# Kernel optimization log

Hardware: AMD Instinct MI355X
Metric: run time of the kernel (lower is better)

## Reference

```python
import jax, jax.numpy as jnp
import numpy as np

L, C, H, FF = 12, 768, 12, 3072
DH = C // H
VOCAB = 30522
B, P, T = 64, 196, 40
PATCH_FLAT = 768  # 16*16*3
MAXP, MAXW = P + 1, T + 2


def _ln(x, w, b, eps):
    m = jnp.mean(x, axis=-1, keepdims=True)
    v = jnp.mean(jnp.square(x - m), axis=-1, keepdims=True)
    return (x - m) * jax.lax.rsqrt(v + eps) * w + b


def setup_inputs() -> dict:
    key = jax.random.key(0)
    ks = iter(jax.random.split(key, 40))
    s = 0.02
    rn = lambda shape: jax.random.normal(next(ks), shape, jnp.float32) * s
    return {
        'vis_in': jax.random.normal(next(ks), (B, P, PATCH_FLAT), jnp.float32),
        'txt_in': jax.random.randint(next(ks), (B, T), 0, VOCAB),
        'vis_mask': jnp.ones((B, P), jnp.int32),
        'txt_mask': jnp.ones((B, T), jnp.int32),
        'patch_w': rn((C, PATCH_FLAT)), 'patch_b': jnp.zeros((C,), jnp.float32),
        'w_embed': rn((VOCAB, C)),
        't_pos': rn((MAXW, C)),
        'v_pos': rn((1, MAXP, C)),
        'v_cls': rn((1, 1, C)),
        'v_mod': rn((1, 1, C)), 't_mod': rn((1, 1, C)),
        'vn_w': jnp.ones((C,), jnp.float32), 'vn_b': jnp.zeros((C,), jnp.float32),
        'tn_w': jnp.ones((C,), jnp.float32), 'tn_b': jnp.zeros((C,), jnp.float32),
        'qkv_w': rn((L, 3 * C, C)), 'qkv_b': jnp.zeros((L, 3 * C), jnp.float32),
        'proj_w': rn((L, C, C)), 'proj_b': jnp.zeros((L, C), jnp.float32),
        'n1_w': jnp.ones((L, C), jnp.float32), 'n1_b': jnp.zeros((L, C), jnp.float32),
        'n2_w': jnp.ones((L, C), jnp.float32), 'n2_b': jnp.zeros((L, C), jnp.float32),
        'fc1_w': rn((L, FF, C)), 'fc1_b': jnp.zeros((L, FF), jnp.float32),
        'fc2_w': rn((L, C, FF)), 'fc2_b': jnp.zeros((L, C), jnp.float32),
    }


def reference(vis_in, txt_in, vis_mask, txt_mask, patch_w, patch_b, w_embed, t_pos,
              v_pos, v_cls, v_mod, t_mod, vn_w, vn_b, tn_w, tn_b, qkv_w, qkv_b,
              proj_w, proj_b, n1_w, n1_b, n2_w, n2_b, fc1_w, fc1_b, fc2_w, fc2_b):
    Bsz = vis_in.shape[0]
    # patch projection and word embedding
    v_emb = vis_in @ patch_w.T + patch_b                      # [B, P, C]
    t_emb = w_embed[txt_in]                                    # [B, T, C]
    v_emb = jnp.concatenate([jnp.broadcast_to(v_cls, (Bsz, 1, C)), v_emb], axis=1)
    VL = v_emb.shape[1]                                        # P + 1
    v_emb = _ln(v_emb + v_pos[:, :VL] + v_mod, vn_w, vn_b, 1e-5)
    t_emb = _ln(t_emb + t_pos[:T] + t_mod, tn_w, tn_b, 1e-5)
    x = jnp.concatenate([t_emb, v_emb], axis=1)                # [B, N, C], N = T+1+P
    m = jnp.concatenate([txt_mask, jnp.ones((Bsz, 1), txt_mask.dtype), vis_mask], axis=-1)
    # pairwise mask: attn_mask[b,i,j] == 0 -> masked (broadcast over heads)
    masked = (m[:, None, :, None] * m[:, None, None, :]) == 0  # [B,1,N,N]
    scale = DH ** -0.5
    for l in range(L):
        h = _ln(x, n1_w[l], n1_b[l], 1e-6)
        qkv = (h @ qkv_w[l].T + qkv_b[l]).reshape(Bsz, -1, 3, H, DH)
        q = jnp.transpose(qkv[:, :, 0], (0, 2, 1, 3))          # [B,H,N,DH]
        k = jnp.transpose(qkv[:, :, 1], (0, 2, 1, 3))
        v = jnp.transpose(qkv[:, :, 2], (0, 2, 1, 3))
        attn = jnp.einsum('bhqd,bhkd->bhqk', q, k) * scale
        attn = jnp.where(masked, jnp.asarray(-1e30, attn.dtype), attn)
        attn = jax.nn.softmax(attn, axis=-1)
        o = jnp.einsum('bhqk,bhkd->bhqd', attn, v)
        o = jnp.transpose(o, (0, 2, 1, 3)).reshape(Bsz, -1, C)
        x = x + (o @ proj_w[l].T + proj_b[l])
        h2 = _ln(x, n2_w[l], n2_b[l], 1e-6)
        h2 = jax.nn.gelu(h2 @ fc1_w[l].T + fc1_b[l], approximate=False)
        x = x + (h2 @ fc2_w[l].T + fc2_b[l])
    return x
```

## Files before the change

### kernel.cpp

```cpp
#include <hip/hip_runtime.h>
#include <hip/hip_bf16.h>

using bf16 = __hip_bfloat16;
typedef __bf16 bfv8 __attribute__((ext_vector_type(8)));
typedef float f32x4 __attribute__((ext_vector_type(4)));

#define DEVI __device__ __forceinline__

constexpr int L_ = 12, C_ = 768, H_ = 12, FF_ = 3072, DH_ = 64;
constexpr int B_ = 64, P_ = 196, T_ = 40;
constexpr int N_ = T_ + 1 + P_;
constexpr int M_ = B_ * N_;
constexpr int MPAD = 15360;
constexpr int NKV = 256;
constexpr int BP_ = B_ * P_;

constexpr size_t OFF_X   = 0;
constexpr size_t SZ_X    = (size_t)MPAD * C_ * 4;
constexpr size_t OFF_H   = OFF_X + SZ_X;
constexpr size_t SZ_H    = (size_t)MPAD * C_ * 2;
constexpr size_t OFF_Q   = OFF_H + SZ_H;
constexpr size_t SZ_QKV1 = (size_t)B_ * H_ * NKV * DH_ * 2;
constexpr size_t OFF_K   = OFF_Q + SZ_QKV1;
constexpr size_t OFF_V   = OFF_K + SZ_QKV1;
constexpr size_t OFF_O   = OFF_V + SZ_QKV1;
constexpr size_t SZ_O    = SZ_H;
constexpr size_t OFF_FFH = OFF_O + SZ_O;
constexpr size_t SZ_FFH  = (size_t)MPAD * FF_ * 2;
constexpr size_t OFF_WB  = OFF_FFH + SZ_FFH;
constexpr size_t SZ_WB   = (size_t)(2304 + 768 + 3072 + 3072) * 768 * 2;
constexpr size_t WS_NEED = OFF_WB + SZ_WB;
constexpr size_t OFF_PTMP = OFF_FFH;
constexpr size_t OFF_VISB = OFF_FFH + (size_t)40 * 1024 * 1024;
constexpr size_t OFF_PWB  = OFF_WB;

DEVI void gld_lds16(const bf16* g, bf16* l) {
  __builtin_amdgcn_global_load_lds((__attribute__((address_space(1))) void*)(g),
                                   (__attribute__((address_space(3))) void*)(l), 16, 0, 0);
}

DEVI void swz_tiles(int bid, int G, int NTC, int& bm, int& bn) {
  const int qq = G >> 3, rr = G & 7;
  const int xcd = bid & 7, base = bid >> 3;
  const int lin = (xcd < rr ? xcd * (qq + 1) : rr * (qq + 1) + (xcd - rr) * qq) + base;
  bm = lin / NTC;
  bn = lin - bm * NTC;
}

DEVI uint packbf(float lo, float hi) {
  union { struct { bf16 x, y; } h; uint u; } r;
  r.h.x = __float2bfloat16(lo); r.h.y = __float2bfloat16(hi);
  return r.u;
}

DEVI float gelu_f(float v) {
  const float p = v * (1.5957691f + 0.07135481f * v * v) * 1.442695041f;
  const float d = exp2f(-p);
  return v / (1.f + d);
}

template <int EPI>
__global__ __launch_bounds__(256) void gemm_mb(
    const bf16* __restrict__ A, const bf16* __restrict__ W,
    const float* __restrict__ bias, float* __restrict__ outf,
    float* __restrict__ outf2, bf16* __restrict__ outb,
    bf16* __restrict__ qb, bf16* __restrict__ kb, bf16* __restrict__ vb,
    int Nout, int K, int Mvalid, int NTC) {
  __shared__ alignas(16) bf16 As[2][128 * 32];
  __shared__ alignas(16) bf16 Bs[2][128 * 32];

  const int tid = threadIdx.x, wid = tid >> 6, lane = tid & 63;
  const int wm = wid >> 1, wn = wid & 1;
  int bm, bn;
  swz_tiles(blockIdx.x, gridDim.x, NTC, bm, bn);
  const size_t arow0 = (size_t)bm * 128;
  const size_t brow0 = (size_t)bn * 128;

  const int srow = tid >> 2;
  const int gch = ((tid & 3) - ((tid >> 3) & 3)) & 3;
  const bf16* pa0 = A + (arow0 + srow) * K + gch * 8;
  const bf16* pa1 = A + (arow0 + 64 + srow) * K + gch * 8;
  const bf16* pb0 = W + (brow0 + srow) * K + gch * 8;
  const bf16* pb1 = W + (brow0 + 64 + srow) * K + gch * 8;
  bf16* da0[2] = {&As[0][(wid * 16) * 32], &As[1][(wid * 16) * 32]};
  bf16* da1[2] = {&As[0][(64 + wid * 16) * 32], &As[1][(64 + wid * 16) * 32]};
  bf16* db0[2] = {&Bs[0][(wid * 16) * 32], &Bs[1][(wid * 16) * 32]};
  bf16* db1[2] = {&Bs[0][(64 + wid * 16) * 32], &Bs[1][(64 + wid * 16) * 32]};

  auto STAGE = [&](int t, int b) {
    const size_t k = (size_t)t * 32;
    gld_lds16(pa0 + k, da0[b]);
    gld_lds16(pa1 + k, da1[b]);
    gld_lds16(pb0 + k, db0[b]);
    gld_lds16(pb1 + k, db1[b]);
  };

  f32x4 acc[4][4];
#pragma unroll
  for (int m = 0; m < 4; m++)
#pragma unroll
    for (int n = 0; n < 4; n++) acc[m][n] = (f32x4){0.f, 0.f, 0.f, 0.f};

  const int la = lane & 15, g = lane >> 4;
  const int slot8 = ((g + (la >> 1)) & 3) * 8;

  const int NT = K >> 5;
  STAGE(0, 0);
  for (int t = 0; t < NT; ++t) {
    const int b = t & 1;
    if (t + 1 < NT) {
      STAGE(t + 1, b ^ 1);
      asm volatile("s_waitcnt vmcnt(4)" ::: "memory");
    } else {
      asm volatile("s_waitcnt vmcnt(0)" ::: "memory");
    }
    asm volatile("s_barrier" ::: "memory");
    bfv8 af[4], bfr[4];
#pragma unroll
    for (int n = 0; n < 4; n++)
      bfr[n] = *(const bfv8*)&Bs[b][(wn * 64 + n * 16 + la) * 32 + slot8];
#pragma unroll
    for (int m = 0; m < 4; m++)
      af[m] = *(const bfv8*)&As[b][(wm * 64 + m * 16 + la) * 32 + slot8];
#pragma unroll
    for (int m = 0; m < 4; m++)
#pragma unroll
      for (int n = 0; n < 4; n++)
        acc[m][n] = __builtin_amdgcn_mfma_f32_16x16x32_bf16(af[m], bfr[n], acc[m][n], 0, 0, 0);
    asm volatile("s_barrier" ::: "memory");
  }

  const int row0 = (int)arow0 + wm * 64;
  const int col0 = (int)brow0 + wn * 64;
  float bv[4];
#pragma unroll
  for (int n = 0; n < 4; n++) bv[n] = bias[col0 + n * 16 + la];

  if constexpr (EPI == 0 || EPI == 2 || EPI == 4) {
#pragma unroll
    for (int n = 0; n < 4; n++) {
      const int colb = col0 + n * 16 + la;
#pragma unroll
      for (int m = 0; m < 4; m++)
#pragma unroll
        for (int j = 0; j < 4; j++) {
          const int row = row0 + m * 16 + g * 4 + j;
          const float v = acc[m][n][j] + bv[n];
          if constexpr (EPI == 0) outf[(size_t)row * Nout + colb] = v;
          else if constexpr (EPI == 2) outf[(size_t)row * Nout + colb] += v;
          else { if (row < Mvalid) outf2[(size_t)row * Nout + colb] = outf[(size_t)row * Nout + colb] + v; }
        }
    }
  } else if constexpr (EPI == 3) {
#pragma unroll
    for (int m = 0; m < 4; m++)
#pragma unroll
      for (int j = 0; j < 4; j++) {
        const int row = row0 + m * 16 + g * 4 + j;
#pragma unroll
        for (int n = 0; n < 4; n++) {
          const float v = gelu_f(acc[m][n][j] + bv[n]);
          const float p = __shfl_xor(v, 1);
          if (!(lane & 1))
            *(uint*)(outb + (size_t)row * Nout + col0 + n * 16 + la) = packbf(v, p);
        }
      }
  } else {
#pragma unroll
    for (int m = 0; m < 4; m++)
#pragma unroll
      for (int j = 0; j < 4; j++) {
        const int row = row0 + m * 16 + g * 4 + j;
        const bool ok = row < Mvalid;
        const int bI = row / N_;
        const int nI = row - bI * N_;
#pragma unroll
        for (int n = 0; n < 4; n++) {
          const int colb = col0 + n * 16 + la;
          const float v = acc[m][n][j] + bv[n];
          const float p = __shfl_xor(v, 1);
          if (ok && !(lane & 1)) {
            const int s = colb / C_;
            const int rem = colb - s * C_;
            const int hh = rem >> 6, dd = rem & 63;
            bf16* dst = (s == 0) ? qb : (s == 1) ? kb : vb;
            *(uint*)(dst + (((size_t)bI * H_ + hh) * NKV + nI) * DH_ + dd) = packbf(v, p);
          }
        }
      }
  }
}

__global__ __launch_bounds__(256) void conv_weights_k(
    const float* __restrict__ wq, const float* __restrict__ wp,
    const float* __restrict__ wf1, const float* __restrict__ wf2,
    bf16* __restrict__ dst) {
  const long n0 = 2304L * 768 / 4, n1 = 768L * 768 / 4;
  const long n2 = 3072L * 768 / 4;
  const long tot = n0 + n1 + 2 * n2;
  for (long i = (long)blockIdx.x * 256 + threadIdx.x; i < tot; i += (long)gridDim.x * 256) {
    const float* s; long off;
    if (i < n0) { s = wq; off = i; }
    else if (i < n0 + n1) { s = wp; off = i - n0; }
    else if (i < n0 + n1 + n2) { s = wf1; off = i - n0 - n1; }
    else { s = wf2; off = i - n0 - n1 - n2; }
    float4 v = ((const float4*)s)[off];
    union { short4 q; bf16 h[4]; } u;
    u.h[0] = __float2bfloat16(v.x); u.h[1] = __float2bfloat16(v.y);
    u.h[2] = __float2bfloat16(v.z); u.h[3] = __float2bfloat16(v.w);
    ((short4*)dst)[i] = u.q;
  }
}

__global__ __launch_bounds__(256) void f32_to_bf16_k(const float* __restrict__ s,
                                                     bf16* __restrict__ d, long n4) {
  long i = (long)blockIdx.x * 256 + threadIdx.x;
  long stride = (long)gridDim.x * 256;
  for (; i < n4; i += stride) {
    float4 v = ((const float4*)s)[i];
    union { short4 q; bf16 h[4]; } u;
    u.h[0] = __float2bfloat16(v.x); u.h[1] = __float2bfloat16(v.y);
    u.h[2] = __float2bfloat16(v.z); u.h[3] = __float2bfloat16(v.w);
    ((short4*)d)[i] = u.q;
  }
}

__global__ __launch_bounds__(256) void embed_kernel(
    const float* __restrict__ ptmp, const int* __restrict__ txt_in,
    const float* __restrict__ wemb, const float* __restrict__ tpos,
    const float* __restrict__ vpos, const float* __restrict__ vcls,
    const float* __restrict__ vmod, const float* __restrict__ tmod,
    const float* __restrict__ vnw, const float* __restrict__ vnb,
    const float* __restrict__ tnw, const float* __restrict__ tnb,
    float* __restrict__ x) {
  const int row = blockIdx.x;
  const int tid = threadIdx.x;
  if (row >= M_) {
    for (int i = tid; i < C_; i += 256) x[(size_t)row * C_ + i] = 0.f;
    return;
  }
  const int b = row / N_, n = row - (row / N_) * N_;
  const bool istxt = n < T_;
  float e[3];
#pragma unroll
  for (int i = 0; i < 3; i++) {
    const int c = tid + i * 256;
    float v;
    if (istxt) {
      v = wemb[(size_t)txt_in[b * T_ + n] * C_ + c] + tpos[n * C_ + c] + tmod[c];
    } else {
      const int vi = n - T_;
      const float base = (vi == 0) ? vcls[c] : ptmp[((size_t)b * P_ + (vi - 1)) * C_ + c];
      v = base + vpos[vi * C_ + c] + vmod[c];
    }
    e[i] = v;
  }
  float s = e[0] + e[1] + e[2];
  float s2 = e[0] * e[0] + e[1] * e[1] + e[2] * e[2];
#pragma unroll
  for (int d = 1; d < 64; d <<= 1) { s += __shfl_xor(s, d); s2 += __shfl_xor(s2, d); }
  __shared__ float rs[4], rs2[4];
  const int wid = tid >> 6, lane = tid & 63;
  if (lane == 0) { rs[wid] = s; rs2[wid] = s2; }
  __syncthreads();
  s = rs[0] + rs[1] + rs[2] + rs[3];
  s2 = rs2[0] + rs2[1] + rs2[2] + rs2[3];
  const float mean = s * (1.f / C_);
  const float var = s2 * (1.f / C_) - mean * mean;
  const float rr = rsqrtf(var + 1e-5f);
  const float* w = istxt ? tnw : vnw;
  const float* bb = istxt ? tnb : vnb;
#pragma unroll
  for (int i = 0; i < 3; i++) {
    const int c = tid + i * 256;
    x[(size_t)row * C_ + c] = (e[i] - mean) * rr * w[c] + bb[c];
  }
}

__global__ __launch_bounds__(256) void ln_rows(const float* __restrict__ x,
                                               const float* __restrict__ w,
                                               const float* __restrict__ b,
                                               bf16* __restrict__ out, float eps) {
  const int row = blockIdx.x * 4 + (threadIdx.x >> 6);
  const int lane = threadIdx.x & 63;
  if (row >= MPAD) return;
  bf16* op = out + (size_t)row * C_;
  if (row >= M_) {
#pragma unroll
    for (int i = 0; i < 3; i++)
      *(short4*)(op + (lane + 64 * i) * 4) = make_short4(0, 0, 0, 0);
    return;
  }
  const float4* xp = (const float4*)(x + (size_t)row * C_);
  float4 v[3];
  float s = 0.f, s2 = 0.f;
#pragma unroll
  for (int i = 0; i < 3; i++) {
    v[i] = xp[lane + 64 * i];
    s += v[i].x + v[i].y + v[i].z + v[i].w;
    s2 += v[i].x * v[i].x + v[i].y * v[i].y + v[i].z * v[i].z + v[i].w * v[i].w;
  }
#pragma unroll
  for (int d = 1; d < 64; d <<= 1) { s += __shfl_xor(s, d); s2 += __shfl_xor(s2, d); }
  const float mean = s * (1.f / C_);
  const float rr = rsqrtf(s2 * (1.f / C_) - mean * mean + eps);
#pragma unroll
  for (int i = 0; i < 3; i++) {
    const int c0 = (lane + 64 * i) * 4;
    const float4 w4 = *(const float4*)(w + c0);
    const float4 b4 = *(const float4*)(b + c0);
    union { short4 s4; bf16 h[4]; } u;
    u.h[0] = __float2bfloat16((v[i].x - mean) * rr * w4.x + b4.x);
    u.h[1] = __float2bfloat16((v[i].y - mean) * rr * w4.y + b4.y);
    u.h[2] = __float2bfloat16((v[i].z - mean) * rr * w4.z + b4.z);
    u.h[3] = __float2bfloat16((v[i].w - mean) * rr * w4.w + b4.w);
    *(short4*)(op + c0) = u.s4;
  }
}

DEVI float maskval(const int* __restrict__ tm, const int* __restrict__ vm, int b, int j) {
  if (j < T_) return tm[b * T_ + j] ? 1.f : 0.f;
  if (j == T_) return 1.f;
  if (j < N_) return vm[b * P_ + (j - T_ - 1)] ? 1.f : 0.f;
  return 0.f;
}

__global__ __launch_bounds__(256) void attn_fused(
    const bf16* __restrict__ qb, const bf16* __restrict__ kb,
    const bf16* __restrict__ vb, const int* __restrict__ txt_mask,
    const int* __restrict__ vis_mask, bf16* __restrict__ ob) {
  __shared__ alignas(16) __bf16 Vt[64 * 264];
  __shared__ alignas(16) __bf16 Ps[64 * 264];
  const int qblk = blockIdx.x;
  const int bh = blockIdx.y;
  const int b = bh / H_, hh = bh - b * H_;
  const int tid = threadIdx.x, wid = tid >> 6, lane = tid & 63;

  const __bf16* Vg = (const __bf16*)(vb + (size_t)bh * NKV * DH_);
#pragma unroll
  for (int it = 0; it < 8; it++) {
    const int r = lane + 64 * (it & 3);
    const int c8 = (wid + 4 * (it >> 2)) * 8;
    bfv8 v;
    if (r < N_) v = *(const bfv8*)(Vg + (size_t)r * DH_ + c8);
    else { union { int4 i; bfv8 x; } z; z.i = make_int4(0,0,0,0); v = z.x; }
#pragma unroll
    for (int d = 0; d < 8; d++) Vt[(c8 + d) * 264 + r] = v[d];
  }

  const int qbase = qblk * 64 + wid * 16;
  const __bf16* Qg = (const __bf16*)(qb + (size_t)bh * NKV * DH_);
  const __bf16* Kg = (const __bf16*)(kb + (size_t)bh * NKV * DH_);
  bfv8 aq[2];
#pragma unroll
  for (int kk = 0; kk < 2; kk++)
    aq[kk] = *(const bfv8*)(Qg + (size_t)(qbase + (lane & 15)) * DH_ + kk * 32 + (lane >> 4) * 8);

  f32x4 acc[16];
#pragma unroll
  for (int f = 0; f < 16; f++) acc[f] = (f32x4){0.f, 0.f, 0.f, 0.f};
#pragma unroll
  for (int f = 0; f < 16; f++) {
#pragma unroll
    for (int kk = 0; kk < 2; kk++) {
      bfv8 bk = *(const bfv8*)(Kg + (size_t)(f * 16 + (lane & 15)) * DH_ + kk * 32 + (lane >> 4) * 8);
      acc[f] = __builtin_amdgcn_mfma_f32_16x16x32_bf16(aq[kk], bk, acc[f], 0, 0, 0);
    }
  }

  float cm[16];
#pragma unroll
  for (int f = 0; f < 16; f++)
    cm[f] = maskval(txt_mask, vis_mask, b, f * 16 + (lane & 15));

  const float scale = 0.125f;
#pragma unroll
  for (int j = 0; j < 4; j++) {
    const int qr = qbase + (lane >> 4) * 4 + j;
    const float qm = (qr < N_) ? maskval(txt_mask, vis_mask, b, qr) : 1.f;
    float sv[16];
    float mx = -3.0e38f;
#pragma unroll
    for (int f = 0; f < 16; f++) {
      const int col = f * 16 + (lane & 15);
      float sc;
      if (col >= N_) sc = -INFINITY;
      else if (qm * cm[f] == 0.f) sc = -1e30f;
      else sc = acc[f][j] * scale;
      sv[f] = sc;
      mx = fmaxf(mx, sc);
    }
#pragma unroll
    for (int d = 1; d < 16; d <<= 1) mx = fmaxf(mx, __shfl_xor(mx, d));
    float sum = 0.f;
#pragma unroll
    for (int f = 0; f < 16; f++) { const float p = expf(sv[f] - mx); sv[f] = p; sum += p; }
#pragma unroll
    for (int d = 1; d < 16; d <<= 1) sum += __shfl_xor(sum, d);
    const float inv = 1.f / sum;
    const int ql = wid * 16 + (lane >> 4) * 4 + j;
#pragma unroll
    for (int f = 0; f < 16; f++)
      Ps[ql * 264 + f * 16 + (lane & 15)] = (__bf16)(sv[f] * inv);
  }

  __syncthreads();

  f32x4 oacc[4];
#pragma unroll
  for (int n = 0; n < 4; n++) oacc[n] = (f32x4){0.f, 0.f, 0.f, 0.f};
#pragma unroll
  for (int kk = 0; kk < 8; kk++) {
    bfv8 ap = *(const bfv8*)&Ps[(wid * 16 + (lane & 15)) * 264 + kk * 32 + (lane >> 4) * 8];
#pragma unroll
    for (int n = 0; n < 4; n++) {
      bfv8 bv = *(const bfv8*)&Vt[(n * 16 + (lane & 15)) * 264 + kk * 32 + (lane >> 4) * 8];
      oacc[n] = __builtin_amdgcn_mfma_f32_16x16x32_bf16(ap, bv, oacc[n], 0, 0, 0);
    }
  }
#pragma unroll
  for (int n = 0; n < 4; n++)
#pragma unroll
    for (int j = 0; j < 4; j++) {
      const int q = qbase + (lane >> 4) * 4 + j;
      if (q < N_)
        ob[((size_t)b * N_ + q) * C_ + hh * 64 + n * 16 + (lane & 15)] =
            __float2bfloat16(oacc[n][j]);
    }
}

extern "C" void kernel_launch(void* const* d_in, const int* in_sizes, int n_in,
                              void* d_out, int out_size, void* d_ws, size_t ws_size,
                              hipStream_t stream) {
  const float* vis_in  = (const float*)d_in[0];
  const int*   txt_in  = (const int*)d_in[1];
  const int*   vis_mask = (const int*)d_in[2];
  const int*   txt_mask = (const int*)d_in[3];
  const float* patch_w = (const float*)d_in[4];
  const float* patch_b = (const float*)d_in[5];
  const float* w_embed = (const float*)d_in[6];
  const float* t_pos   = (const float*)d_in[7];
  const float* v_pos   = (const float*)d_in[8];
  const float* v_cls   = (const float*)d_in[9];
  const float* v_mod   = (const float*)d_in[10];
  const float* t_mod   = (const float*)d_in[11];
  const float* vn_w = (const float*)d_in[12];
  const float* vn_b = (const float*)d_in[13];
  const float* tn_w = (const float*)d_in[14];
  const float* tn_b = (const float*)d_in[15];
  const float* qkv_w = (const float*)d_in[16];
  const float* qkv_b = (const float*)d_in[17];
  const float* proj_w = (const float*)d_in[18];
  const float* proj_b = (const float*)d_in[19];
  const float* n1_w = (const float*)d_in[20];
  const float* n1_b = (const float*)d_in[21];
  const float* n2_w = (const float*)d_in[22];
  const float* n2_b = (const float*)d_in[23];
  const float* fc1_w = (const float*)d_in[24];
  const float* fc1_b = (const float*)d_in[25];
  const float* fc2_w = (const float*)d_in[26];
  const float* fc2_b = (const float*)d_in[27];

  char* ws = (char*)d_ws;
  if (ws_size < WS_NEED) {
    hipMemsetAsync(d_out, 0, (size_t)out_size * 4, stream);
    return;
  }
  float* x    = (float*)(ws + OFF_X);
  bf16* h     = (bf16*)(ws + OFF_H);
  bf16* qbuf  = (bf16*)(ws + OFF_Q);
  bf16* kbuf  = (bf16*)(ws + OFF_K);
  bf16* vbuf  = (bf16*)(ws + OFF_V);
  bf16* obuf  = (bf16*)(ws + OFF_O);
  bf16* ffh   = (bf16*)(ws + OFF_FFH);
  bf16* wq    = (bf16*)(ws + OFF_WB);
  bf16* wp    = wq + (size_t)2304 * 768;
  bf16* wf1   = wp + (size_t)768 * 768;
  bf16* wf2   = wf1 + (size_t)3072 * 768;
  float* ptmp = (float*)(ws + OFF_PTMP);
  bf16* visb  = (bf16*)(ws + OFF_VISB);
  bf16* pwb   = (bf16*)(ws + OFF_PWB);

  f32_to_bf16_k<<<1024, 256, 0, stream>>>(vis_in, visb, (long)BP_ * C_ / 4);
  f32_to_bf16_k<<<256, 256, 0, stream>>>(patch_w, pwb, (long)C_ * C_ / 4);
  gemm_mb<0><<<(BP_ / 128) * (C_ / 128), 256, 0, stream>>>(
      visb, pwb, patch_b, ptmp, nullptr, nullptr, nullptr, nullptr, nullptr,
      C_, C_, BP_, C_ / 128);
  embed_kernel<<<MPAD, 256, 0, stream>>>(ptmp, txt_in, w_embed, t_pos, v_pos, v_cls,
                                         v_mod, t_mod, vn_w, vn_b, tn_w, tn_b, x);

  for (int l = 0; l < L_; l++) {
    conv_weights_k<<<2048, 256, 0, stream>>>(
        qkv_w + (size_t)l * 2304 * 768, proj_w + (size_t)l * 768 * 768,
        fc1_w + (size_t)l * 3072 * 768, fc2_w + (size_t)l * 768 * 3072, wq);

    ln_rows<<<MPAD / 4, 256, 0, stream>>>(x, n1_w + l * C_, n1_b + l * C_, h, 1e-6f);
    gemm_mb<1><<<(MPAD / 128) * (2304 / 128), 256, 0, stream>>>(
        h, wq, qkv_b + (size_t)l * 2304, nullptr, nullptr, nullptr, qbuf, kbuf, vbuf,
        2304, C_, M_, 2304 / 128);
    attn_fused<<<dim3(4, B_ * H_), 256, 0, stream>>>(qbuf, kbuf, vbuf, txt_mask,
                                                     vis_mask, obuf);
    gemm_mb<2><<<(MPAD / 128) * (C_ / 128), 256, 0, stream>>>(
        obuf, wp, proj_b + (size_t)l * C_, x, nullptr, nullptr, nullptr, nullptr,
        nullptr, C_, C_, M_, C_ / 128);
    ln_rows<<<MPAD / 4, 256, 0, stream>>>(x, n2_w + l * C_, n2_b + l * C_, h, 1e-6f);
    gemm_mb<3><<<(MPAD / 128) * (FF_ / 128), 256, 0, stream>>>(
        h, wf1, fc1_b + (size_t)l * FF_, nullptr, nullptr, ffh, nullptr, nullptr,
        nullptr, FF_, C_, M_, FF_ / 128);
    if (l < L_ - 1) {
      gemm_mb<2><<<(MPAD / 128) * (C_ / 128), 256, 0, stream>>>(
          ffh, wf2, fc2_b + (size_t)l * C_, x, nullptr, nullptr, nullptr, nullptr,
          nullptr, C_, FF_, M_, C_ / 128);
    } else {
      gemm_mb<4><<<(MPAD / 128) * (C_ / 128), 256, 0, stream>>>(
          ffh, wf2, fc2_b + (size_t)l * C_, x, (float*)d_out, nullptr, nullptr,
          nullptr, nullptr, C_, FF_, M_, C_ / 128);
    }
  }
}
```

Before: 6.019 ms.

## Replace 128x128 GEMM with 256x256 8-wave pipelined tile kernel

```diff
diff --git a/kernel.cpp b/kernel.cpp
--- a/kernel.cpp
+++ b/kernel.cpp
@@ -60,77 +60,118 @@
 }
 
 template <int EPI>
-__global__ __launch_bounds__(256) void gemm_mb(
+__global__ __launch_bounds__(512, 2) void gemm8q(
     const bf16* __restrict__ A, const bf16* __restrict__ W,
     const float* __restrict__ bias, float* __restrict__ outf,
     float* __restrict__ outf2, bf16* __restrict__ outb,
     bf16* __restrict__ qb, bf16* __restrict__ kb, bf16* __restrict__ vb,
     int Nout, int K, int Mvalid, int NTC) {
-  __shared__ alignas(16) bf16 As[2][128 * 32];
-  __shared__ alignas(16) bf16 Bs[2][128 * 32];
+  extern __shared__ __align__(16) char lds[];
+  constexpr int BUFSZ = 65536;
+  constexpr int BOFF  = 32768;
 
   const int tid = threadIdx.x, wid = tid >> 6, lane = tid & 63;
-  const int wm = wid >> 1, wn = wid & 1;
+  const int wm = wid >> 2, wn = wid & 3;
   int bm, bn;
   swz_tiles(blockIdx.x, gridDim.x, NTC, bm, bn);
-  const size_t arow0 = (size_t)bm * 128;
-  const size_t brow0 = (size_t)bn * 128;
-
-  const int srow = tid >> 2;
-  const int gch = ((tid & 3) - ((tid >> 3) & 3)) & 3;
-  const bf16* pa0 = A + (arow0 + srow) * K + gch * 8;
-  const bf16* pa1 = A + (arow0 + 64 + srow) * K + gch * 8;
-  const bf16* pb0 = W + (brow0 + srow) * K + gch * 8;
-  const bf16* pb1 = W + (brow0 + 64 + srow) * K + gch * 8;
-  bf16* da0[2] = {&As[0][(wid * 16) * 32], &As[1][(wid * 16) * 32]};
-  bf16* da1[2] = {&As[0][(64 + wid * 16) * 32], &As[1][(64 + wid * 16) * 32]};
-  bf16* db0[2] = {&Bs[0][(wid * 16) * 32], &Bs[1][(wid * 16) * 32]};
-  bf16* db1[2] = {&Bs[0][(64 + wid * 16) * 32], &Bs[1][(64 + wid * 16) * 32]};
-
-  auto STAGE = [&](int t, int b) {
-    const size_t k = (size_t)t * 32;
-    gld_lds16(pa0 + k, da0[b]);
-    gld_lds16(pa1 + k, da1[b]);
-    gld_lds16(pb0 + k, db0[b]);
-    gld_lds16(pb1 + k, db1[b]);
+  const size_t arow0 = (size_t)bm * 256;
+  const size_t brow0 = (size_t)bn * 256;
+
+  const int lrow = lane >> 3;
+  const int xr = ((lane & 7) ^ lrow) * 8;
+  const bf16* Ag = A + (arow0 + wid * 16 + lrow) * K + xr;
+  const bf16* Wg = W + (brow0 + wid * 16 + lrow) * K + xr;
+
+  auto STG = [&](int isA, int h, int t, int P) {
+    char* base = lds + P * BUFSZ + (isA ? 0 : BOFF) + h * 16384 + wid * 2048;
+    const bf16* g = (isA ? Ag : Wg) + (size_t)(h * 128) * K + t * 64;
+    gld_lds16(g, (bf16*)base);
+    gld_lds16(g + (size_t)8 * K, (bf16*)(base + 1024));
   };
 
-  f32x4 acc[4][4];
-#pragma unroll
-  for (int m = 0; m < 4; m++)
+  const int la = lane & 15, g4 = lane >> 4;
+  const int s7 = lane & 7;
+
+  f32x4 acc[8][4];
+#pragma unroll
+  for (int m = 0; m < 8; m++)
 #pragma unroll
     for (int n = 0; n < 4; n++) acc[m][n] = (f32x4){0.f, 0.f, 0.f, 0.f};
 
-  const int la = lane & 15, g = lane >> 4;
-  const int slot8 = ((g + (la >> 1)) & 3) * 8;
-
-  const int NT = K >> 5;
-  STAGE(0, 0);
-  for (int t = 0; t < NT; ++t) {
-    const int b = t & 1;
-    if (t + 1 < NT) {
-      STAGE(t + 1, b ^ 1);
-      asm volatile("s_waitcnt vmcnt(4)" ::: "memory");
-    } else {
-      asm volatile("s_waitcnt vmcnt(0)" ::: "memory");
-    }
-    asm volatile("s_barrier" ::: "memory");
-    bfv8 af[4], bfr[4];
-#pragma unroll
-    for (int n = 0; n < 4; n++)
-      bfr[n] = *(const bfv8*)&Bs[b][(wn * 64 + n * 16 + la) * 32 + slot8];
-#pragma unroll
-    for (int m = 0; m < 4; m++)
-      af[m] = *(const bfv8*)&As[b][(wm * 64 + m * 16 + la) * 32 + slot8];
-#pragma unroll
-    for (int m = 0; m < 4; m++)
-#pragma unroll
-      for (int n = 0; n < 4; n++)
-        acc[m][n] = __builtin_amdgcn_mfma_f32_16x16x32_bf16(af[m], bfr[n], acc[m][n], 0, 0, 0);
-    asm volatile("s_barrier" ::: "memory");
-  }
-
-  const int row0 = (int)arow0 + wm * 64;
+  bfv8 af[4][2], bfr[4][2];
+
+  auto DSRA = [&](int P, int mo) {
+    const char* ab = lds + P * BUFSZ + wm * 16384;
+#pragma unroll
+    for (int mi = 0; mi < 4; mi++) {
+      const int r = (mo + mi) * 16 + la;
+#pragma unroll
+      for (int ks = 0; ks < 2; ks++)
+        af[mi][ks] = *(const bfv8*)(ab + r * 128 + (((ks * 4 + g4) ^ s7) * 16));
+    }
+  };
+  auto DSRB = [&](int P, int no) {
+    const char* bb = lds + P * BUFSZ + BOFF + (wn >> 1) * 16384;
+#pragma unroll
+    for (int ni = 0; ni < 2; ni++) {
+      const int c = (wn & 1) * 64 + (no + ni) * 16 + la;
+#pragma unroll
+      for (int ks = 0; ks < 2; ks++)
+        bfr[no + ni][ks] = *(const bfv8*)(bb + c * 128 + (((ks * 4 + g4) ^ s7) * 16));
+    }
+  };
+  auto QM = [&](int mo, int no) {
+    __builtin_amdgcn_s_setprio(1);
+#pragma unroll
+    for (int ks = 0; ks < 2; ks++)
+#pragma unroll
+      for (int mi = 0; mi < 4; mi++)
+#pragma unroll
+        for (int ni = 0; ni < 2; ni++)
+          acc[mo + mi][no + ni] = __builtin_amdgcn_mfma_f32_16x16x32_bf16(
+              af[mi][ks], bfr[no + ni][ks], acc[mo + mi][no + ni], 0, 0, 0);
+    __builtin_amdgcn_s_setprio(0);
+  };
+
+#define BARR asm volatile("s_barrier" ::: "memory")
+
+  const int NT = K >> 6;
+  const int NI = NT >> 1;
+
+  STG(1, 0, 0, 0); STG(1, 1, 0, 0); STG(0, 0, 0, 0); STG(0, 1, 0, 0);
+  STG(0, 0, 1, 1); STG(0, 1, 1, 1);
+  asm volatile("s_waitcnt vmcnt(4)" ::: "memory");
+  BARR;
+
+  for (int i = 0; i < NI; i++) {
+    const int t = 2 * i;
+    const bool p2 = (t + 2 < NT), p3 = (t + 3 < NT);
+    DSRA(0, 0); DSRB(0, 0); STG(1, 0, t + 1, 1);
+    BARR; QM(0, 0); BARR;
+    DSRB(0, 2); STG(1, 1, t + 1, 1);
+    BARR; QM(0, 2); BARR;
+    DSRA(0, 4); if (p2) STG(0, 0, t + 2, 0);
+    BARR; QM(4, 0); BARR;
+    if (p2) STG(0, 1, t + 2, 0);
+    BARR; QM(4, 2);
+    if (p2) { asm volatile("s_waitcnt vmcnt(4)" ::: "memory"); }
+    else    { asm volatile("s_waitcnt vmcnt(0)" ::: "memory"); }
+    BARR;
+    DSRA(1, 0); DSRB(1, 0); if (p2) STG(1, 0, t + 2, 0);
+    BARR; QM(0, 0); BARR;
+    DSRB(1, 2); if (p2) STG(1, 1, t + 2, 0);
+    BARR; QM(0, 2); BARR;
+    DSRA(1, 4); if (p3) STG(0, 0, t + 3, 1);
+    BARR; QM(4, 0); BARR;
+    if (p3) STG(0, 1, t + 3, 1);
+    BARR; QM(4, 2);
+    if (p3) { asm volatile("s_waitcnt vmcnt(4)" ::: "memory"); }
+    else    { asm volatile("s_waitcnt vmcnt(0)" ::: "memory"); }
+    BARR;
+  }
+#undef BARR
+
+  const int row0 = (int)arow0 + wm * 128;
   const int col0 = (int)brow0 + wn * 64;
   float bv[4];
 #pragma unroll
@@ -141,10 +182,10 @@
     for (int n = 0; n < 4; n++) {
       const int colb = col0 + n * 16 + la;
 #pragma unroll
-      for (int m = 0; m < 4; m++)
+      for (int m = 0; m < 8; m++)
 #pragma unroll
         for (int j = 0; j < 4; j++) {
-          const int row = row0 + m * 16 + g * 4 + j;
+          const int row = row0 + m * 16 + g4 * 4 + j;
           const float v = acc[m][n][j] + bv[n];
           if constexpr (EPI == 0) outf[(size_t)row * Nout + colb] = v;
           else if constexpr (EPI == 2) outf[(size_t)row * Nout + colb] += v;
@@ -153,10 +194,10 @@
     }
   } else if constexpr (EPI == 3) {
 #pragma unroll
-    for (int m = 0; m < 4; m++)
+    for (int m = 0; m < 8; m++)
 #pragma unroll
       for (int j = 0; j < 4; j++) {
-        const int row = row0 + m * 16 + g * 4 + j;
+        const int row = row0 + m * 16 + g4 * 4 + j;
 #pragma unroll
         for (int n = 0; n < 4; n++) {
           const float v = gelu_f(acc[m][n][j] + bv[n]);
@@ -167,10 +208,10 @@
       }
   } else {
 #pragma unroll
-    for (int m = 0; m < 4; m++)
+    for (int m = 0; m < 8; m++)
 #pragma unroll
       for (int j = 0; j < 4; j++) {
-        const int row = row0 + m * 16 + g * 4 + j;
+        const int row = row0 + m * 16 + g4 * 4 + j;
         const bool ok = row < Mvalid;
         const int bI = row / N_;
         const int nI = row - bI * N_;
@@ -481,11 +522,18 @@
   bf16* visb  = (bf16*)(ws + OFF_VISB);
   bf16* pwb   = (bf16*)(ws + OFF_PWB);
 
+  constexpr int LDSQ = 131072;
+  (void)hipFuncSetAttribute((const void*)gemm8q<0>, hipFuncAttributeMaxDynamicSharedMemorySize, LDSQ);
+  (void)hipFuncSetAttribute((const void*)gemm8q<1>, hipFuncAttributeMaxDynamicSharedMemorySize, LDSQ);
+  (void)hipFuncSetAttribute((const void*)gemm8q<2>, hipFuncAttributeMaxDynamicSharedMemorySize, LDSQ);
+  (void)hipFuncSetAttribute((const void*)gemm8q<3>, hipFuncAttributeMaxDynamicSharedMemorySize, LDSQ);
+  (void)hipFuncSetAttribute((const void*)gemm8q<4>, hipFuncAttributeMaxDynamicSharedMemorySize, LDSQ);
+
   f32_to_bf16_k<<<1024, 256, 0, stream>>>(vis_in, visb, (long)BP_ * C_ / 4);
   f32_to_bf16_k<<<256, 256, 0, stream>>>(patch_w, pwb, (long)C_ * C_ / 4);
-  gemm_mb<0><<<(BP_ / 128) * (C_ / 128), 256, 0, stream>>>(
+  gemm8q<0><<<(BP_ / 256) * (C_ / 256), 512, LDSQ, stream>>>(
       visb, pwb, patch_b, ptmp, nullptr, nullptr, nullptr, nullptr, nullptr,
-      C_, C_, BP_, C_ / 128);
+      C_, C_, BP_, C_ / 256);
   embed_kernel<<<MPAD, 256, 0, stream>>>(ptmp, txt_in, w_embed, t_pos, v_pos, v_cls,
                                          v_mod, t_mod, vn_w, vn_b, tn_w, tn_b, x);
 
@@ -495,26 +543,26 @@
         fc1_w + (size_t)l * 3072 * 768, fc2_w + (size_t)l * 768 * 3072, wq);
 
     ln_rows<<<MPAD / 4, 256, 0, stream>>>(x, n1_w + l * C_, n1_b + l * C_, h, 1e-6f);
-    gemm_mb<1><<<(MPAD / 128) * (2304 / 128), 256, 0, stream>>>(
+    gemm8q<1><<<(MPAD / 256) * (2304 / 256), 512, LDSQ, stream>>>(
         h, wq, qkv_b + (size_t)l * 2304, nullptr, nullptr, nullptr, qbuf, kbuf, vbuf,
-        2304, C_, M_, 2304 / 128);
+        2304, C_, M_, 2304 / 256);
     attn_fused<<<dim3(4, B_ * H_), 256, 0, stream>>>(qbuf, kbuf, vbuf, txt_mask,
                                                      vis_mask, obuf);
-    gemm_mb<2><<<(MPAD / 128) * (C_ / 128), 256, 0, stream>>>(
+    gemm8q<2><<<(MPAD / 256) * (C_ / 256), 512, LDSQ, stream>>>(
         obuf, wp, proj_b + (size_t)l * C_, x, nullptr, nullptr, nullptr, nullptr,
-        nullptr, C_, C_, M_, C_ / 128);
+        nullptr, C_, C_, M_, C_ / 256);
     ln_rows<<<MPAD / 4, 256, 0, stream>>>(x, n2_w + l * C_, n2_b + l * C_, h, 1e-6f);
-    gemm_mb<3><<<(MPAD / 128) * (FF_ / 128), 256, 0, stream>>>(
+    gemm8q<3><<<(MPAD / 256) * (FF_ / 256), 512, LDSQ, stream>>>(
         h, wf1, fc1_b + (size_t)l * FF_, nullptr, nullptr, ffh, nullptr, nullptr,
-        nullptr, FF_, C_, M_, FF_ / 128);
+        nullptr, FF_, C_, M_, FF_ / 256);
     if (l < L_ - 1) {
-      gemm_mb<2><<<(MPAD / 128) * (C_ / 128), 256, 0, stream>>>(
+      gemm8q<2><<<(MPAD / 256) * (C_ / 256), 512, LDSQ, stream>>>(
           ffh, wf2, fc2_b + (size_t)l * C_, x, nullptr, nullptr, nullptr, nullptr,
-          nullptr, C_, FF_, M_, C_ / 128);
+          nullptr, C_, FF_, M_, C_ / 256);
     } else {
-      gemm_mb<4><<<(MPAD / 128) * (C_ / 128), 256, 0, stream>>>(
+      gemm8q<4><<<(MPAD / 256) * (C_ / 256), 512, LDSQ, stream>>>(
           ffh, wf2, fc2_b + (size_t)l * C_, x, (float*)d_out, nullptr, nullptr,
-          nullptr, nullptr, C_, FF_, M_, C_ / 128);
-    }
-  }
-}
+          nullptr, nullptr, C_, FF_, M_, C_ / 256);
+    }
+  }
+}
```

Measured after the change: 6.353 ms. 1.06x slower.
